# Kernel tuning notes

Measured on AMD Instinct MI355X. Metric: run time of the kernel, lower is better.

## Reference

```python
import jax, jax.numpy as jnp
import numpy as np

E, T, I, O = 8, 8192, 2048, 4096  # experts, total_tokens, in_features, out_features


def setup_inputs() -> dict:
    key = jax.random.key(0)
    k1, k2, k3 = jax.random.split(key, 3)
    inputs = jax.random.normal(k1, (T, I), dtype=jnp.float32)
    # lecun_normal-style scale for the (E, I, O) kernel (fan_in = I)
    kernel = jax.random.normal(k2, (E, I, O), dtype=jnp.float32) * (1.0 / np.float32(np.sqrt(I)))
    # nonzero bias so the ragged bias-expansion path is exercised
    bias = jax.random.normal(k3, (E, O), dtype=jnp.float32) * 0.02
    # tokens are sorted by expert; equal groups summing exactly to T
    group_sizes = jnp.full((E,), T // E, dtype=jnp.int32)
    return {"inputs": inputs, "group_sizes": group_sizes, "kernel": kernel, "bias": bias}


def reference(inputs, group_sizes, kernel, bias):
    # Ragged grouped GEMM: row block g of `inputs` (size group_sizes[g]) is
    # multiplied by kernel[g] of shape (I, O). Matches _ragged_dot with
    # out_first=False: contraction dims ((1,), (1,)), rhs group dim 0.
    out = jax.lax.ragged_dot(inputs, kernel, group_sizes)  # (T, O)
    # Per-group bias add: bias[e] broadcast over that expert's token block.
    expert_ids = jnp.repeat(jnp.arange(E), group_sizes, total_repeat_length=T)
    return out + bias[expert_ids]
```

## Files before the change

### kernel.cpp

```cpp
#include <hip/hip_runtime.h>


typedef short bf16x8 __attribute__((ext_vector_type(8)));
typedef float f32x4 __attribute__((ext_vector_type(4)));
typedef unsigned short u16x8 __attribute__((ext_vector_type(8)));

constexpr int Ecnt = 8;
constexpr int Ttok = 8192;
constexpr int Ifeat = 2048;
constexpr int Ofeat = 4096;
constexpr int BM = 128, BN = 128, BK = 64;

__device__ __forceinline__ unsigned short f2bf(float f) {
  unsigned u = __float_as_uint(f);
  unsigned r = (u + 0x7FFFu + ((u >> 16) & 1u)) >> 16;
  return (unsigned short)r;
}

__global__ __launch_bounds__(256) void cvt_a(const float* __restrict__ src,
                                             unsigned short* __restrict__ dst) {
  size_t i = ((size_t)blockIdx.x * 256 + threadIdx.x) * 8;
  float4 f0 = *(const float4*)(src + i);
  float4 f1 = *(const float4*)(src + i + 4);
  u16x8 v;
  v[0] = f2bf(f0.x); v[1] = f2bf(f0.y); v[2] = f2bf(f0.z); v[3] = f2bf(f0.w);
  v[4] = f2bf(f1.x); v[5] = f2bf(f1.y); v[6] = f2bf(f1.z); v[7] = f2bf(f1.w);
  *(u16x8*)(dst + i) = v;
}

__global__ __launch_bounds__(256) void cvt_b(const float* __restrict__ src,
                                             unsigned short* __restrict__ dst) {
  constexpr int LDST = 129;
  __shared__ float tile[64 * LDST];
  const int e = blockIdx.z;
  const int i0 = blockIdx.y * 64;
  const int o0 = blockIdx.x * 128;
  const int tid = threadIdx.x;
  {
    const int tx = tid & 31, ty = tid >> 5;
    const float* s = src + ((size_t)e * Ifeat + i0) * Ofeat + o0 + tx * 4;
#pragma unroll
    for (int r = 0; r < 8; ++r) {
      int i = r * 8 + ty;
      float4 f = *(const float4*)(s + (size_t)i * Ofeat);
      float* l = tile + i * LDST + tx * 4;
      l[0] = f.x; l[1] = f.y; l[2] = f.z; l[3] = f.w;
    }
  }
  __syncthreads();
  {
    const int ic = (tid & 7) * 8;
    const int oc = tid >> 3;
#pragma unroll
    for (int p = 0; p < 4; ++p) {
      int o = p * 32 + oc;
      u16x8 v;
#pragma unroll
      for (int j = 0; j < 8; ++j) v[j] = f2bf(tile[(ic + j) * LDST + o]);
      unsigned short* d =
          dst + ((size_t)e * Ofeat + o0 + o) * Ifeat + i0 + ic;
      *(u16x8*)d = v;
    }
  }
}

__device__ __forceinline__ void ld16(const unsigned short* g, unsigned short* l) {
  __builtin_amdgcn_global_load_lds(
      (const __attribute__((address_space(1))) unsigned int*)g,
      (__attribute__((address_space(3))) unsigned int*)l, 16, 0, 0);
}

__global__ __launch_bounds__(256) void moe_gemm(
    const unsigned short* __restrict__ A,
    const unsigned short* __restrict__ Bt,
    const int* __restrict__ gs,
    const float* __restrict__ bias,
    float* __restrict__ C) {
  __shared__ unsigned short lA[BM * BK];
  __shared__ unsigned short lB[BN * BK];

  const int tid = threadIdx.x;
  const int bid = blockIdx.x;
  const int xcd = bid & 7;
  const int j = bid >> 3;
  const int ct = xcd * 4 + (j >> 6);
  const int rtile = j & 63;
  const int row0 = rtile * BM;
  const int col0 = ct * BN;

  int e = 0;
  {
    int cum = 0;
#pragma unroll
    for (int g = 0; g < Ecnt; ++g) {
      int s = gs[g];
      if (row0 >= cum + s) { cum += s; e = g + 1; }
    }
  }

  const unsigned short* Ag = A + (size_t)row0 * Ifeat;
  const unsigned short* Bg = Bt + ((size_t)e * Ofeat + col0) * Ifeat;

  const int wave = tid >> 6, lane = tid & 63;
  const int wm = (wave >> 1) * 64, wn = (wave & 1) * 64;
  const int lrow = lane & 15;
  const int kg = lane >> 4;
  const int xr = lrow & 7;

  const int64_t koff[4] = {
      (int64_t)((tid + 0) >> 3) * Ifeat + (((tid + 0) & 7) ^ (((tid + 0) >> 3) & 7)) * 8,
      (int64_t)((tid + 256) >> 3) * Ifeat + (((tid + 256) & 7) ^ (((tid + 256) >> 3) & 7)) * 8,
      (int64_t)((tid + 512) >> 3) * Ifeat + (((tid + 512) & 7) ^ (((tid + 512) >> 3) & 7)) * 8,
      (int64_t)((tid + 768) >> 3) * Ifeat + (((tid + 768) & 7) ^ (((tid + 768) >> 3) & 7)) * 8};
  const unsigned short* asrc[4] = {Ag + koff[0], Ag + koff[1], Ag + koff[2],
                                   Ag + koff[3]};
  const unsigned short* bsrc[4] = {Bg + koff[0], Bg + koff[1], Bg + koff[2],
                                   Bg + koff[3]};
  unsigned short* adst[4] = {lA + (size_t)tid * 8, lA + (size_t)(tid + 256) * 8,
                             lA + (size_t)(tid + 512) * 8,
                             lA + (size_t)(tid + 768) * 8};
  unsigned short* bdst[4] = {lB + (size_t)tid * 8, lB + (size_t)(tid + 256) * 8,
                             lB + (size_t)(tid + 512) * 8,
                             lB + (size_t)(tid + 768) * 8};

  f32x4 acc[4][4];
#pragma unroll
  for (int i = 0; i < 4; ++i)
#pragma unroll
    for (int jj = 0; jj < 4; ++jj) acc[i][jj] = (f32x4){0.f, 0.f, 0.f, 0.f};

  for (int k0 = 0; k0 < Ifeat; k0 += BK) {
#pragma unroll
    for (int p = 0; p < 4; ++p) ld16(asrc[p] + k0, adst[p]);
#pragma unroll
    for (int p = 0; p < 4; ++p) ld16(bsrc[p] + k0, bdst[p]);
    __syncthreads();

#pragma unroll
    for (int s = 0; s < 2; ++s) {
      bf16x8 af[4], bf[4];
#pragma unroll
      for (int mt = 0; mt < 4; ++mt) {
        const int r = wm + mt * 16 + lrow;
        const int slot = (s * 4 + kg) ^ xr;
        af[mt] = *(const bf16x8*)(lA + r * BK + slot * 8);
      }
#pragma unroll
      for (int nt = 0; nt < 4; ++nt) {
        const int r = wn + nt * 16 + lrow;
        const int slot = (s * 4 + kg) ^ xr;
        bf[nt] = *(const bf16x8*)(lB + r * BK + slot * 8);
      }
#pragma unroll
      for (int mt = 0; mt < 4; ++mt)
#pragma unroll
        for (int nt = 0; nt < 4; ++nt)
          acc[mt][nt] = __builtin_amdgcn_mfma_f32_16x16x32_bf16(
              af[mt], bf[nt], acc[mt][nt], 0, 0, 0);
    }

    __syncthreads();
  }

  const int r0 = (lane >> 4) * 4;
  const int cc = lane & 15;
  const float* be = bias + (size_t)e * Ofeat;
#pragma unroll
  for (int mt = 0; mt < 4; ++mt) {
    const int row = row0 + wm + mt * 16 + r0;
#pragma unroll
    for (int nt = 0; nt < 4; ++nt) {
      const int col = col0 + wn + nt * 16 + cc;
      const float b = be[col];
      float* Cp = C + (size_t)row * Ofeat + col;
#pragma unroll
      for (int r = 0; r < 4; ++r) Cp[(size_t)r * Ofeat] = acc[mt][nt][r] + b;
    }
  }
}

extern "C" void kernel_launch(void* const* d_in, const int* in_sizes, int n_in,
                              void* d_out, int out_size, void* d_ws, size_t ws_size,
                              hipStream_t stream) {
  const float* inputs = (const float*)d_in[0];
  const int* group_sizes = (const int*)d_in[1];
  const float* kern = (const float*)d_in[2];
  const float* bias = (const float*)d_in[3];
  float* out = (float*)d_out;

  unsigned short* Abf = (unsigned short*)d_ws;
  unsigned short* Bbf = Abf + (size_t)Ttok * Ifeat;

  cvt_a<<<(Ttok * (size_t)Ifeat) / (8 * 256), 256, 0, stream>>>(inputs, Abf);
  cvt_b<<<dim3(Ofeat / 128, Ifeat / 64, Ecnt), 256, 0, stream>>>(kern, Bbf);

  moe_gemm<<<Ttok / BM * (Ofeat / BN), 256, 0, stream>>>(Abf, Bbf, group_sizes,
                                                         bias, out);
}
```

Baseline: 630.1 us.

## Assign GEMM tiles dynamically per XCD via atomic queues for L2 locality

Each GEMM block no longer derives its tile from blockIdx. It reads its hardware XCC id and pulls a tile from that XCD's atomic work queue, stealing from other queues once its own is empty. Each queue covers 8 row tiles (one expert's rows) across all column tiles, so blocks running on one XCD share the same B expert slice and A rows in their private L2. The cost is a memset launch, one atomic and a barrier per block, plus a dependence on the XCC register value.

```diff
diff --git a/kernel.cpp b/kernel.cpp
--- a/kernel.cpp
+++ b/kernel.cpp
@@ -10,6 +10,8 @@
 constexpr int Ifeat = 2048;
 constexpr int Ofeat = 4096;
 constexpr int BM = 128, BN = 128, BK = 64;
+constexpr int NTILE = (Ttok / BM) * (Ofeat / BN);
+constexpr int QCAP = NTILE / 8;
 
 __device__ __forceinline__ unsigned short f2bf(float f) {
   unsigned u = __float_as_uint(f);
@@ -75,17 +77,33 @@
     const unsigned short* __restrict__ Bt,
     const int* __restrict__ gs,
     const float* __restrict__ bias,
-    float* __restrict__ C) {
+    float* __restrict__ C,
+    int* __restrict__ qcnt) {
   __shared__ unsigned short lA[BM * BK];
   __shared__ unsigned short lB[BN * BK];
+  __shared__ int s_tile;
 
   const int tid = threadIdx.x;
-  const int bid = blockIdx.x;
-  const int xcd = bid & 7;
-  const int j = bid >> 3;
-  const int ct = xcd * 4 + (j >> 6);
-  const int rtile = j & 63;
-  const int row0 = rtile * BM;
+
+  if (tid == 0) {
+    unsigned xcc = __builtin_amdgcn_s_getreg(63508) & 7;
+    int t = 0;
+#pragma unroll
+    for (int a = 0; a < 8; ++a) {
+      int q = (xcc + a) & 7;
+      int idx = atomicAdd(&qcnt[q], 1);
+      if (idx < QCAP) { t = (q << 8) | idx; break; }
+    }
+    s_tile = t;
+  }
+  __syncthreads();
+
+  const int tcode = s_tile;
+  const int q = tcode >> 8;
+  const int idx = tcode & 255;
+  const int rt = q * 8 + (idx & 7);
+  const int ct = idx >> 3;
+  const int row0 = rt * BM;
   const int col0 = ct * BN;
 
   int e = 0;
@@ -190,10 +208,12 @@
 
   unsigned short* Abf = (unsigned short*)d_ws;
   unsigned short* Bbf = Abf + (size_t)Ttok * Ifeat;
+  const size_t cnt_off = (size_t)Ttok * Ifeat * 2 + (size_t)Ecnt * Ofeat * Ifeat * 2;
+  int* qcnt = (int*)((char*)d_ws + cnt_off);
 
   cvt_a<<<(Ttok * (size_t)Ifeat) / (8 * 256), 256, 0, stream>>>(inputs, Abf);
   cvt_b<<<dim3(Ofeat / 128, Ifeat / 64, Ecnt), 256, 0, stream>>>(kern, Bbf);
-
-  moe_gemm<<<Ttok / BM * (Ofeat / BN), 256, 0, stream>>>(Abf, Bbf, group_sizes,
-                                                         bias, out);
-}
+  hipMemsetAsync(qcnt, 0, 8 * sizeof(int), stream);
+
+  moe_gemm<<<NTILE, 256, 0, stream>>>(Abf, Bbf, group_sizes, bias, out, qcnt);
+}
```

New measurement: 629.1 us. No clear change (-0.1%).
